# Kernel tuning notes

Hardware: AMD Instinct MI355X
Metric: run time of the kernel (lower is better)

## Reference

```python
import jax, jax.numpy as jnp
import numpy as np

N, T, C, K = 32, 1024, 512, 64
EPS = 1e-12  # torch F.normalize eps


def _l2norm(v, axis):
    n = jnp.sqrt(jnp.sum(v * v, axis=axis, keepdims=True))
    return v / jnp.maximum(n, EPS)


def setup_inputs() -> dict:
    key = jax.random.key(0)
    k1, k2 = jax.random.split(key)
    x = jax.random.normal(k1, (N, T, C), dtype=jnp.float32)
    centroids = jax.random.uniform(k2, (K, C), dtype=jnp.float32)
    # mirrors _init_params: conv.weight = 0.2*centroids, conv.bias = -0.1*||centroids||
    W = 0.2 * centroids
    b = -0.1 * jnp.sqrt(jnp.sum(centroids * centroids, axis=1))
    return {"x": x, "W": W, "b": b, "centroids": centroids}


def reference(x, W, b, centroids):
    # x: [N, T, C] -> [N, C, T]
    xt = jnp.transpose(x, (0, 2, 1))
    # 1x1 Conv1d == per-timestep linear: logits [N, K, T]
    logits = jnp.einsum('kc,nct->nkt', W, xt) + b[None, :, None]
    a = jax.nn.softmax(logits, axis=1)  # softmax over clusters
    # vlad[n,k,c] = sum_t a[n,k,t] * (x[n,c,t] - centroid[k,c])
    #            = (a @ x^T) - sum_t(a) * centroid  (GEMM form, same math)
    vlad = jnp.einsum('nkt,nct->nkc', a, xt) - a.sum(axis=-1)[:, :, None] * centroids[None]
    vlad = _l2norm(vlad, axis=2)          # intra-normalization per cluster
    vlad = vlad.reshape(vlad.shape[0], -1)
    vlad = _l2norm(vlad, axis=1)          # global L2 normalization
    return vlad
```

## Files before the change

### kernel.cpp

```cpp
#include <hip/hip_runtime.h>
#include <cmath>

namespace {

constexpr int N = 32, T = 1024, C = 512, K = 64;
constexpr float EPS = 1e-12f;

typedef short s8v __attribute__((ext_vector_type(8)));
typedef short s4v __attribute__((ext_vector_type(4)));
typedef float f4v __attribute__((ext_vector_type(4)));

__device__ inline unsigned short f2bh(float f) {
  __bf16 h = (__bf16)f;
  return __builtin_bit_cast(unsigned short, h);
}
__device__ inline float bh2f(unsigned short u) {
  __bf16 h = __builtin_bit_cast(__bf16, u);
  return (float)h;
}

#define MFMA16(A, B, Cc) __builtin_amdgcn_mfma_f32_16x16x32_bf16((A), (B), (Cc), 0, 0, 0)

__global__ __launch_bounds__(256, 4) void k_gemm1(
    const float* __restrict__ x, const float* __restrict__ W,
    const float* __restrict__ b, float* __restrict__ aT,
    float* __restrict__ asum_part) {
  __shared__ __align__(16) unsigned short sm[4 * 64 * 72];
  __shared__ float asum_l[256];
  unsigned short* xh_s = sm;
  unsigned short* xl_s = sm + 64 * 72;
  unsigned short* wh_s = sm + 2 * 64 * 72;
  unsigned short* wl_s = sm + 3 * 64 * 72;

  const int tid = threadIdx.x;
  const int w = tid >> 6, lane = tid & 63, lm = lane & 15, lq = lane >> 4;
  const int th = w >> 1;
  const int kh = w & 1;
  const long r0 = (long)blockIdx.x * 64;
  const int n = blockIdx.x >> 4, tl = blockIdx.x & 15;

  f4v acc[2][2] = {};
  float4 px[4], pw[4];
#pragma unroll
  for (int r = 0; r < 4; ++r) {
    const int f = tid + r * 256, t = f >> 4, cg = f & 15;
    px[r] = *(const float4*)&x[(r0 + t) * C + cg * 4];
    pw[r] = *(const float4*)&W[(long)t * C + cg * 4];
  }

  for (int c0 = 0; c0 < C; c0 += 64) {
    __syncthreads();
#pragma unroll
    for (int r = 0; r < 4; ++r) {
      const int f = tid + r * 256, t = f >> 4, cg = f & 15;
      const float ex[4] = {px[r].x, px[r].y, px[r].z, px[r].w};
      const float ew[4] = {pw[r].x, pw[r].y, pw[r].z, pw[r].w};
      s4v xh, xl, wh, wl;
#pragma unroll
      for (int i = 0; i < 4; ++i) {
        unsigned short hb = f2bh(ex[i]);
        xh[i] = (short)hb; xl[i] = (short)f2bh(ex[i] - bh2f(hb));
        hb = f2bh(ew[i]);
        wh[i] = (short)hb; wl[i] = (short)f2bh(ew[i] - bh2f(hb));
      }
      *(s4v*)&xh_s[t * 72 + cg * 4] = xh;
      *(s4v*)&xl_s[t * 72 + cg * 4] = xl;
      *(s4v*)&wh_s[t * 72 + cg * 4] = wh;
      *(s4v*)&wl_s[t * 72 + cg * 4] = wl;
    }
    if (c0 + 64 < C) {
#pragma unroll
      for (int r = 0; r < 4; ++r) {
        const int f = tid + r * 256, t = f >> 4, cg = f & 15;
        px[r] = *(const float4*)&x[(r0 + t) * C + c0 + 64 + cg * 4];
        pw[r] = *(const float4*)&W[(long)t * C + c0 + 64 + cg * 4];
      }
    }
    __syncthreads();

#pragma unroll
    for (int ks = 0; ks < 2; ++ks) {
      const int col = ks * 32 + lq * 8;
      s8v ah[2], al[2], bh[2], bl[2];
#pragma unroll
      for (int i = 0; i < 2; ++i) {
        ah[i] = *(const s8v*)&xh_s[(th * 32 + i * 16 + lm) * 72 + col];
        al[i] = *(const s8v*)&xl_s[(th * 32 + i * 16 + lm) * 72 + col];
        bh[i] = *(const s8v*)&wh_s[(kh * 32 + i * 16 + lm) * 72 + col];
        bl[i] = *(const s8v*)&wl_s[(kh * 32 + i * 16 + lm) * 72 + col];
      }
#pragma unroll
      for (int i = 0; i < 2; ++i)
#pragma unroll
        for (int j = 0; j < 2; ++j) {
          acc[i][j] = MFMA16(ah[i], bh[j], acc[i][j]);
          acc[i][j] = MFMA16(ah[i], bl[j], acc[i][j]);
          acc[i][j] = MFMA16(al[i], bh[j], acc[i][j]);
        }
    }
  }
  __syncthreads();

  float* Ls = (float*)sm;
  float* Ls2 = (float*)(sm + 8704);
  const float bias[2] = {b[kh * 32 + lm], b[kh * 32 + 16 + lm]};
#pragma unroll
  for (int i = 0; i < 2; ++i)
#pragma unroll
    for (int j = 0; j < 2; ++j)
#pragma unroll
      for (int r = 0; r < 4; ++r)
        Ls[(th * 32 + i * 16 + lq * 4 + r) * 68 + kh * 32 + j * 16 + lm] =
            acc[i][j][r] + bias[j];
  __syncthreads();

  {
    const int row = tid >> 2, q = tid & 3;
    float av[16];
#pragma unroll
    for (int u = 0; u < 4; ++u)
      *(float4*)&av[u * 4] = *(const float4*)&Ls[row * 68 + q * 16 + u * 4];
    float m = av[0];
#pragma unroll
    for (int i = 1; i < 16; ++i) m = fmaxf(m, av[i]);
    m = fmaxf(m, __shfl_xor(m, 1, 64));
    m = fmaxf(m, __shfl_xor(m, 2, 64));
    float sum = 0.f;
#pragma unroll
    for (int i = 0; i < 16; ++i) {
      av[i] = __expf(av[i] - m);
      sum += av[i];
    }
    sum += __shfl_xor(sum, 1, 64);
    sum += __shfl_xor(sum, 2, 64);
    const float inv = 1.f / sum;
    float ps[16];
#pragma unroll
    for (int i = 0; i < 16; ++i) {
      av[i] *= inv;
      ps[i] = av[i];
      Ls2[(q * 16 + i) * 68 + row] = av[i];
    }
#pragma unroll
    for (int s = 4; s < 64; s <<= 1)
#pragma unroll
      for (int i = 0; i < 16; ++i) ps[i] += __shfl_xor(ps[i], s, 64);
    if (lane < 4) {
#pragma unroll
      for (int i = 0; i < 16; ++i) asum_l[w * 64 + q * 16 + i] = ps[i];
    }
  }
  __syncthreads();

  if (tid < 64) {
    asum_part[(n * 16 + tl) * 64 + tid] = asum_l[tid] + asum_l[64 + tid] +
                                          asum_l[128 + tid] + asum_l[192 + tid];
  }
#pragma unroll
  for (int r = 0; r < 4; ++r) {
    const int u = tid + r * 256, k = u >> 4, tg = u & 15;
    *(float4*)&aT[((long)n * K + k) * T + tl * 64 + tg * 4] =
        *(const float4*)&Ls2[k * 68 + tg * 4];
  }
}

__global__ __launch_bounds__(256, 2) void k_gemm2(
    const float* __restrict__ x, const float* __restrict__ aT,
    const float* __restrict__ asum_part, const float* __restrict__ cent,
    float* __restrict__ vlad, float* __restrict__ ssq_part) {
  __shared__ __align__(16) unsigned short sm[4 * 64 * 72];
  __shared__ float asum_l[64];
  __shared__ float ssq_l[128];
  unsigned short* ah_s = sm;
  unsigned short* al_s = sm + 64 * 72;
  unsigned short* xh_s = sm + 2 * 64 * 72;
  unsigned short* xl_s = sm + 3 * 64 * 72;

  const int tid = threadIdx.x;
  const int w = tid >> 6, lane = tid & 63, lm = lane & 15, lq = lane >> 4;
  const int kh = w >> 1;
  const int ch = w & 1;
  const int n = blockIdx.x >> 3, cb = blockIdx.x & 7;
  const int c0 = cb * 64;

  if (tid < 64) {
    float s = 0.f;
#pragma unroll
    for (int tl = 0; tl < 16; ++tl) s += asum_part[(n * 16 + tl) * 64 + tid];
    asum_l[tid] = s;
  }

  f4v acc[2][2] = {};
  float4 pa[4], px[4];
#pragma unroll
  for (int r = 0; r < 4; ++r) {
    const int u = tid + r * 256, k = u >> 4, tg = u & 15;
    pa[r] = *(const float4*)&aT[((long)n * K + k) * T + tg * 4];
  }
  {
    const int cg = tid & 15, tq = tid >> 4;
#pragma unroll
    for (int i = 0; i < 4; ++i)
      px[i] = *(const float4*)&x[((long)n * T + tq * 4 + i) * C + c0 + cg * 4];
  }

  for (int t0 = 0; t0 < T; t0 += 64) {
    __syncthreads();
#pragma unroll
    for (int r = 0; r < 4; ++r) {
      const int u = tid + r * 256, k = u >> 4, tg = u & 15;
      const float e[4] = {pa[r].x, pa[r].y, pa[r].z, pa[r].w};
      s4v h, l;
#pragma unroll
      for (int i = 0; i < 4; ++i) {
        unsigned short hb = f2bh(e[i]);
        h[i] = (short)hb;
        l[i] = (short)f2bh(e[i] - bh2f(hb));
      }
      *(s4v*)&ah_s[k * 72 + tg * 4] = h;
      *(s4v*)&al_s[k * 72 + tg * 4] = l;
    }
    {
      const int cg = tid & 15, tq = tid >> 4, t4 = tq * 4;
      float e[4][4];
#pragma unroll
      for (int i = 0; i < 4; ++i) {
        e[i][0] = px[i].x; e[i][1] = px[i].y;
        e[i][2] = px[i].z; e[i][3] = px[i].w;
      }
#pragma unroll
      for (int cc = 0; cc < 4; ++cc) {
        s4v h, l;
#pragma unroll
        for (int i = 0; i < 4; ++i) {
          unsigned short hb = f2bh(e[i][cc]);
          h[i] = (short)hb;
          l[i] = (short)f2bh(e[i][cc] - bh2f(hb));
        }
        *(s4v*)&xh_s[(cg * 4 + cc) * 72 + t4] = h;
        *(s4v*)&xl_s[(cg * 4 + cc) * 72 + t4] = l;
      }
    }
    if (t0 + 64 < T) {
#pragma unroll
      for (int r = 0; r < 4; ++r) {
        const int u = tid + r * 256, k = u >> 4, tg = u & 15;
        pa[r] = *(const float4*)&aT[((long)n * K + k) * T + t0 + 64 + tg * 4];
      }
      const int cg = tid & 15, tq = tid >> 4;
#pragma unroll
      for (int i = 0; i < 4; ++i)
        px[i] = *(const float4*)&x[((long)n * T + t0 + 64 + tq * 4 + i) * C +
                                   c0 + cg * 4];
    }
    __syncthreads();

#pragma unroll
    for (int ks = 0; ks < 2; ++ks) {
      const int col = ks * 32 + lq * 8;
      s8v ah[2], al[2], bh[2], bl[2];
#pragma unroll
      for (int i = 0; i < 2; ++i) {
        ah[i] = *(const s8v*)&ah_s[(kh * 32 + i * 16 + lm) * 72 + col];
        al[i] = *(const s8v*)&al_s[(kh * 32 + i * 16 + lm) * 72 + col];
        bh[i] = *(const s8v*)&xh_s[(ch * 32 + i * 16 + lm) * 72 + col];
        bl[i] = *(const s8v*)&xl_s[(ch * 32 + i * 16 + lm) * 72 + col];
      }
#pragma unroll
      for (int i = 0; i < 2; ++i)
#pragma unroll
        for (int j = 0; j < 2; ++j) {
          acc[i][j] = MFMA16(ah[i], bh[j], acc[i][j]);
          acc[i][j] = MFMA16(ah[i], bl[j], acc[i][j]);
          acc[i][j] = MFMA16(al[i], bh[j], acc[i][j]);
        }
    }
  }

  float ssq[2][4];
#pragma unroll
  for (int i = 0; i < 2; ++i)
#pragma unroll
    for (int r = 0; r < 4; ++r) ssq[i][r] = 0.f;

#pragma unroll
  for (int i = 0; i < 2; ++i) {
#pragma unroll
    for (int r = 0; r < 4; ++r) {
      const int k = kh * 32 + i * 16 + lq * 4 + r;
      const float as = asum_l[k];
#pragma unroll
      for (int j = 0; j < 2; ++j) {
        const int c = c0 + ch * 32 + j * 16 + lm;
        const float v = acc[i][j][r] - as * cent[(long)k * C + c];
        vlad[((long)n * K + k) * C + c] = v;
        ssq[i][r] += v * v;
      }
    }
  }
#pragma unroll
  for (int i = 0; i < 2; ++i)
#pragma unroll
    for (int r = 0; r < 4; ++r) {
      float s = ssq[i][r];
      s += __shfl_xor(s, 1, 64);
      s += __shfl_xor(s, 2, 64);
      s += __shfl_xor(s, 4, 64);
      s += __shfl_xor(s, 8, 64);
      ssq[i][r] = s;
    }
  if (lm == 0) {
#pragma unroll
    for (int i = 0; i < 2; ++i)
#pragma unroll
      for (int r = 0; r < 4; ++r)
        ssq_l[(kh * 32 + i * 16 + lq * 4 + r) * 2 + ch] = ssq[i][r];
  }
  __syncthreads();
  if (tid < 64)
    ssq_part[(n * 8 + cb) * 64 + tid] = ssq_l[tid * 2] + ssq_l[tid * 2 + 1];
}

__global__ __launch_bounds__(256) void k_norm(
    const float* __restrict__ vlad, const float* __restrict__ ssq_part,
    float* __restrict__ out) {
  __shared__ float denom[64];
  __shared__ float contrib[64];
  __shared__ float ginv;

  const int tid = threadIdx.x;
  const int n = blockIdx.x >> 4;
  const int chunk = blockIdx.x & 15;

  if (tid < 64) {
    float ss = 0.f;
#pragma unroll
    for (int cb = 0; cb < 8; ++cb) ss += ssq_part[(n * 8 + cb) * 64 + tid];
    const float d = fmaxf(sqrtf(ss), EPS);
    denom[tid] = d;
    contrib[tid] = ss / (d * d);
  }
  __syncthreads();
  if (tid == 0) {
    float s = 0.f;
#pragma unroll
    for (int k = 0; k < K; ++k) s += contrib[k];
    ginv = 1.0f / fmaxf(sqrtf(s), EPS);
  }
  __syncthreads();

#pragma unroll
  for (int q = 0; q < 2; ++q) {
    const int f4 = tid + q * 256;
    const long off = chunk * 2048 + (long)f4 * 4;
    const int k = (int)(off >> 9);
    float4 v = *(const float4*)&vlad[(long)n * K * C + off];
    const float sc = ginv / denom[k];
    v.x *= sc; v.y *= sc; v.z *= sc; v.w *= sc;
    *(float4*)&out[(long)n * K * C + off] = v;
  }
}

}

extern "C" void kernel_launch(void* const* d_in, const int* in_sizes, int n_in,
                              void* d_out, int out_size, void* d_ws,
                              size_t ws_size, hipStream_t stream) {
  const float* x = reinterpret_cast<const float*>(d_in[0]);
  const float* W = reinterpret_cast<const float*>(d_in[1]);
  const float* b = reinterpret_cast<const float*>(d_in[2]);
  const float* cent = reinterpret_cast<const float*>(d_in[3]);
  float* out = reinterpret_cast<float*>(d_out);

  float* p = reinterpret_cast<float*>(d_ws);
  float* aTg = p;                 p += (size_t)N * K * T;
  float* vlad = p;                p += (size_t)N * K * C;
  float* asum_part = p;           p += (size_t)512 * 64;
  float* ssq_part = p;

  k_gemm1<<<(N * T) / 64, 256, 0, stream>>>(x, W, b, aTg, asum_part);
  k_gemm2<<<N * 8, 256, 0, stream>>>(x, aTg, asum_part, cent, vlad, ssq_part);
  k_norm<<<N * 16, 256, 0, stream>>>(vlad, ssq_part, out);
}
```

Baseline: 128.7 us.

## Double-buffer LDS with 32-wide K steps in both GEMM kernels

Both GEMM kernels now use two LDS buffers with a 32-element reduction step. Each iteration computes from one buffer while converting and storing the next tile into the other, so only one barrier per step is needed instead of two. In gemm2, thread roles are split so half the threads load x and half load the assignment matrix, which cuts registers per thread. This adds twice as many loop iterations, and gemm1's launch bound drops to 2 blocks per CU, which may reduce occupancy.

```diff
diff --git a/kernel.cpp b/kernel.cpp
--- a/kernel.cpp
+++ b/kernel.cpp
@@ -5,6 +5,8 @@
 
 constexpr int N = 32, T = 1024, C = 512, K = 64;
 constexpr float EPS = 1e-12f;
+constexpr int SR = 40;
+constexpr int PL = 64 * SR;
 
 typedef short s8v __attribute__((ext_vector_type(8)));
 typedef short s4v __attribute__((ext_vector_type(4)));
@@ -18,19 +20,24 @@
   __bf16 h = __builtin_bit_cast(__bf16, u);
   return (float)h;
 }
+__device__ inline void cvt4(const float4 v, s4v& h, s4v& l) {
+  const float e[4] = {v.x, v.y, v.z, v.w};
+#pragma unroll
+  for (int i = 0; i < 4; ++i) {
+    unsigned short hb = f2bh(e[i]);
+    h[i] = (short)hb;
+    l[i] = (short)f2bh(e[i] - bh2f(hb));
+  }
+}
 
 #define MFMA16(A, B, Cc) __builtin_amdgcn_mfma_f32_16x16x32_bf16((A), (B), (Cc), 0, 0, 0)
 
-__global__ __launch_bounds__(256, 4) void k_gemm1(
+__global__ __launch_bounds__(256, 2) void k_gemm1(
     const float* __restrict__ x, const float* __restrict__ W,
     const float* __restrict__ b, float* __restrict__ aT,
     float* __restrict__ asum_part) {
-  __shared__ __align__(16) unsigned short sm[4 * 64 * 72];
+  __shared__ __align__(16) unsigned short sm[2][4 * PL];
   __shared__ float asum_l[256];
-  unsigned short* xh_s = sm;
-  unsigned short* xl_s = sm + 64 * 72;
-  unsigned short* wh_s = sm + 2 * 64 * 72;
-  unsigned short* wl_s = sm + 3 * 64 * 72;
 
   const int tid = threadIdx.x;
   const int w = tid >> 6, lane = tid & 63, lm = lane & 15, lq = lane >> 4;
@@ -40,54 +47,56 @@
   const int n = blockIdx.x >> 4, tl = blockIdx.x & 15;
 
   f4v acc[2][2] = {};
-  float4 px[4], pw[4];
-#pragma unroll
-  for (int r = 0; r < 4; ++r) {
-    const int f = tid + r * 256, t = f >> 4, cg = f & 15;
+  float4 px[2], pw[2];
+
+#pragma unroll
+  for (int r = 0; r < 2; ++r) {
+    const int u = tid + r * 256, t = u >> 3, cg = u & 7;
     px[r] = *(const float4*)&x[(r0 + t) * C + cg * 4];
     pw[r] = *(const float4*)&W[(long)t * C + cg * 4];
   }
-
-  for (int c0 = 0; c0 < C; c0 += 64) {
-    __syncthreads();
-#pragma unroll
-    for (int r = 0; r < 4; ++r) {
-      const int f = tid + r * 256, t = f >> 4, cg = f & 15;
-      const float ex[4] = {px[r].x, px[r].y, px[r].z, px[r].w};
-      const float ew[4] = {pw[r].x, pw[r].y, pw[r].z, pw[r].w};
-      s4v xh, xl, wh, wl;
-#pragma unroll
-      for (int i = 0; i < 4; ++i) {
-        unsigned short hb = f2bh(ex[i]);
-        xh[i] = (short)hb; xl[i] = (short)f2bh(ex[i] - bh2f(hb));
-        hb = f2bh(ew[i]);
-        wh[i] = (short)hb; wl[i] = (short)f2bh(ew[i] - bh2f(hb));
-      }
-      *(s4v*)&xh_s[t * 72 + cg * 4] = xh;
-      *(s4v*)&xl_s[t * 72 + cg * 4] = xl;
-      *(s4v*)&wh_s[t * 72 + cg * 4] = wh;
-      *(s4v*)&wl_s[t * 72 + cg * 4] = wl;
-    }
-    if (c0 + 64 < C) {
-#pragma unroll
-      for (int r = 0; r < 4; ++r) {
-        const int f = tid + r * 256, t = f >> 4, cg = f & 15;
-        px[r] = *(const float4*)&x[(r0 + t) * C + c0 + 64 + cg * 4];
-        pw[r] = *(const float4*)&W[(long)t * C + c0 + 64 + cg * 4];
-      }
-    }
-    __syncthreads();
-
-#pragma unroll
-    for (int ks = 0; ks < 2; ++ks) {
-      const int col = ks * 32 + lq * 8;
+  {
+    unsigned short* xh = sm[0];
+    unsigned short* xl = sm[0] + PL;
+    unsigned short* wh = sm[0] + 2 * PL;
+    unsigned short* wl = sm[0] + 3 * PL;
+#pragma unroll
+    for (int r = 0; r < 2; ++r) {
+      const int u = tid + r * 256, t = u >> 3, cg = u & 7;
+      s4v h, l;
+      cvt4(px[r], h, l);
+      *(s4v*)&xh[t * SR + cg * 4] = h;
+      *(s4v*)&xl[t * SR + cg * 4] = l;
+      cvt4(pw[r], h, l);
+      *(s4v*)&wh[t * SR + cg * 4] = h;
+      *(s4v*)&wl[t * SR + cg * 4] = l;
+    }
+  }
+  __syncthreads();
+
+  for (int it = 0; it < 16; ++it) {
+    const int cur = it & 1;
+    if (it < 15) {
+      const int c0 = (it + 1) * 32;
+#pragma unroll
+      for (int r = 0; r < 2; ++r) {
+        const int u = tid + r * 256, t = u >> 3, cg = u & 7;
+        px[r] = *(const float4*)&x[(r0 + t) * C + c0 + cg * 4];
+        pw[r] = *(const float4*)&W[(long)t * C + c0 + cg * 4];
+      }
+    }
+    {
+      const unsigned short* xh = sm[cur];
+      const unsigned short* xl = sm[cur] + PL;
+      const unsigned short* wh = sm[cur] + 2 * PL;
+      const unsigned short* wl = sm[cur] + 3 * PL;
       s8v ah[2], al[2], bh[2], bl[2];
 #pragma unroll
       for (int i = 0; i < 2; ++i) {
-        ah[i] = *(const s8v*)&xh_s[(th * 32 + i * 16 + lm) * 72 + col];
-        al[i] = *(const s8v*)&xl_s[(th * 32 + i * 16 + lm) * 72 + col];
-        bh[i] = *(const s8v*)&wh_s[(kh * 32 + i * 16 + lm) * 72 + col];
-        bl[i] = *(const s8v*)&wl_s[(kh * 32 + i * 16 + lm) * 72 + col];
+        ah[i] = *(const s8v*)&xh[(th * 32 + i * 16 + lm) * SR + lq * 8];
+        al[i] = *(const s8v*)&xl[(th * 32 + i * 16 + lm) * SR + lq * 8];
+        bh[i] = *(const s8v*)&wh[(kh * 32 + i * 16 + lm) * SR + lq * 8];
+        bl[i] = *(const s8v*)&wl[(kh * 32 + i * 16 + lm) * SR + lq * 8];
       }
 #pragma unroll
       for (int i = 0; i < 2; ++i)
@@ -98,11 +107,28 @@
           acc[i][j] = MFMA16(al[i], bh[j], acc[i][j]);
         }
     }
-  }
-  __syncthreads();
-
-  float* Ls = (float*)sm;
-  float* Ls2 = (float*)(sm + 8704);
+    if (it < 15) {
+      unsigned short* xh = sm[cur ^ 1];
+      unsigned short* xl = sm[cur ^ 1] + PL;
+      unsigned short* wh = sm[cur ^ 1] + 2 * PL;
+      unsigned short* wl = sm[cur ^ 1] + 3 * PL;
+#pragma unroll
+      for (int r = 0; r < 2; ++r) {
+        const int u = tid + r * 256, t = u >> 3, cg = u & 7;
+        s4v h, l;
+        cvt4(px[r], h, l);
+        *(s4v*)&xh[t * SR + cg * 4] = h;
+        *(s4v*)&xl[t * SR + cg * 4] = l;
+        cvt4(pw[r], h, l);
+        *(s4v*)&wh[t * SR + cg * 4] = h;
+        *(s4v*)&wl[t * SR + cg * 4] = l;
+      }
+    }
+    __syncthreads();
+  }
+
+  float* Ls = (float*)&sm[0][0];
+  float* Ls2 = (float*)&sm[1][0];
   const float bias[2] = {b[kh * 32 + lm], b[kh * 32 + 16 + lm]};
 #pragma unroll
   for (int i = 0; i < 2; ++i)
@@ -168,13 +194,9 @@
     const float* __restrict__ x, const float* __restrict__ aT,
     const float* __restrict__ asum_part, const float* __restrict__ cent,
     float* __restrict__ vlad, float* __restrict__ ssq_part) {
-  __shared__ __align__(16) unsigned short sm[4 * 64 * 72];
+  __shared__ __align__(16) unsigned short sm[2][4 * PL];
   __shared__ float asum_l[64];
   __shared__ float ssq_l[128];
-  unsigned short* ah_s = sm;
-  unsigned short* al_s = sm + 64 * 72;
-  unsigned short* xh_s = sm + 2 * 64 * 72;
-  unsigned short* xl_s = sm + 3 * 64 * 72;
 
   const int tid = threadIdx.x;
   const int w = tid >> 6, lane = tid & 63, lm = lane & 15, lq = lane >> 4;
@@ -190,81 +212,81 @@
     asum_l[tid] = s;
   }
 
+  const bool xrole = (tid < 128);
+  const int xcg = tid & 15, xtq = (tid >> 4) & 7;
+  const int au = tid & 127, ak = au >> 1, atg = au & 1;
+
   f4v acc[2][2] = {};
-  float4 pa[4], px[4];
-#pragma unroll
-  for (int r = 0; r < 4; ++r) {
-    const int u = tid + r * 256, k = u >> 4, tg = u & 15;
-    pa[r] = *(const float4*)&aT[((long)n * K + k) * T + tg * 4];
+  float4 p[4];
+
+  if (xrole) {
+#pragma unroll
+    for (int i = 0; i < 4; ++i)
+      p[i] = *(const float4*)&x[((long)n * T + xtq * 4 + i) * C + c0 + xcg * 4];
+  } else {
+#pragma unroll
+    for (int q = 0; q < 4; ++q)
+      p[q] = *(const float4*)&aT[((long)n * K + ak) * T + atg * 16 + q * 4];
   }
   {
-    const int cg = tid & 15, tq = tid >> 4;
-#pragma unroll
-    for (int i = 0; i < 4; ++i)
-      px[i] = *(const float4*)&x[((long)n * T + tq * 4 + i) * C + c0 + cg * 4];
-  }
-
-  for (int t0 = 0; t0 < T; t0 += 64) {
-    __syncthreads();
-#pragma unroll
-    for (int r = 0; r < 4; ++r) {
-      const int u = tid + r * 256, k = u >> 4, tg = u & 15;
-      const float e[4] = {pa[r].x, pa[r].y, pa[r].z, pa[r].w};
-      s4v h, l;
-#pragma unroll
-      for (int i = 0; i < 4; ++i) {
-        unsigned short hb = f2bh(e[i]);
-        h[i] = (short)hb;
-        l[i] = (short)f2bh(e[i] - bh2f(hb));
-      }
-      *(s4v*)&ah_s[k * 72 + tg * 4] = h;
-      *(s4v*)&al_s[k * 72 + tg * 4] = l;
-    }
-    {
-      const int cg = tid & 15, tq = tid >> 4, t4 = tq * 4;
-      float e[4][4];
-#pragma unroll
-      for (int i = 0; i < 4; ++i) {
-        e[i][0] = px[i].x; e[i][1] = px[i].y;
-        e[i][2] = px[i].z; e[i][3] = px[i].w;
-      }
+    unsigned short* ah = sm[0];
+    unsigned short* al = sm[0] + PL;
+    unsigned short* xh = sm[0] + 2 * PL;
+    unsigned short* xl = sm[0] + 3 * PL;
+    if (xrole) {
 #pragma unroll
       for (int cc = 0; cc < 4; ++cc) {
         s4v h, l;
 #pragma unroll
         for (int i = 0; i < 4; ++i) {
-          unsigned short hb = f2bh(e[i][cc]);
+          const float e = ((const float*)&p[i])[cc];
+          unsigned short hb = f2bh(e);
           h[i] = (short)hb;
-          l[i] = (short)f2bh(e[i][cc] - bh2f(hb));
+          l[i] = (short)f2bh(e - bh2f(hb));
         }
-        *(s4v*)&xh_s[(cg * 4 + cc) * 72 + t4] = h;
-        *(s4v*)&xl_s[(cg * 4 + cc) * 72 + t4] = l;
-      }
-    }
-    if (t0 + 64 < T) {
-#pragma unroll
-      for (int r = 0; r < 4; ++r) {
-        const int u = tid + r * 256, k = u >> 4, tg = u & 15;
-        pa[r] = *(const float4*)&aT[((long)n * K + k) * T + t0 + 64 + tg * 4];
-      }
-      const int cg = tid & 15, tq = tid >> 4;
-#pragma unroll
-      for (int i = 0; i < 4; ++i)
-        px[i] = *(const float4*)&x[((long)n * T + t0 + 64 + tq * 4 + i) * C +
-                                   c0 + cg * 4];
-    }
-    __syncthreads();
-
-#pragma unroll
-    for (int ks = 0; ks < 2; ++ks) {
-      const int col = ks * 32 + lq * 8;
+        *(s4v*)&xh[(xcg * 4 + cc) * SR + xtq * 4] = h;
+        *(s4v*)&xl[(xcg * 4 + cc) * SR + xtq * 4] = l;
+      }
+    } else {
+#pragma unroll
+      for (int q = 0; q < 4; ++q) {
+        s4v h, l;
+        cvt4(p[q], h, l);
+        *(s4v*)&ah[ak * SR + atg * 16 + q * 4] = h;
+        *(s4v*)&al[ak * SR + atg * 16 + q * 4] = l;
+      }
+    }
+  }
+  __syncthreads();
+
+  for (int it = 0; it < 32; ++it) {
+    const int cur = it & 1;
+    if (it < 31) {
+      const int t0 = (it + 1) * 32;
+      if (xrole) {
+#pragma unroll
+        for (int i = 0; i < 4; ++i)
+          p[i] = *(const float4*)&x[((long)n * T + t0 + xtq * 4 + i) * C + c0 +
+                                    xcg * 4];
+      } else {
+#pragma unroll
+        for (int q = 0; q < 4; ++q)
+          p[q] =
+              *(const float4*)&aT[((long)n * K + ak) * T + t0 + atg * 16 + q * 4];
+      }
+    }
+    {
+      const unsigned short* ahp = sm[cur];
+      const unsigned short* alp = sm[cur] + PL;
+      const unsigned short* xhp = sm[cur] + 2 * PL;
+      const unsigned short* xlp = sm[cur] + 3 * PL;
       s8v ah[2], al[2], bh[2], bl[2];
 #pragma unroll
       for (int i = 0; i < 2; ++i) {
-        ah[i] = *(const s8v*)&ah_s[(kh * 32 + i * 16 + lm) * 72 + col];
-        al[i] = *(const s8v*)&al_s[(kh * 32 + i * 16 + lm) * 72 + col];
-        bh[i] = *(const s8v*)&xh_s[(ch * 32 + i * 16 + lm) * 72 + col];
-        bl[i] = *(const s8v*)&xl_s[(ch * 32 + i * 16 + lm) * 72 + col];
+        ah[i] = *(const s8v*)&ahp[(kh * 32 + i * 16 + lm) * SR + lq * 8];
+        al[i] = *(const s8v*)&alp[(kh * 32 + i * 16 + lm) * SR + lq * 8];
+        bh[i] = *(const s8v*)&xhp[(ch * 32 + i * 16 + lm) * SR + lq * 8];
+        bl[i] = *(const s8v*)&xlp[(ch * 32 + i * 16 + lm) * SR + lq * 8];
       }
 #pragma unroll
       for (int i = 0; i < 2; ++i)
@@ -275,6 +297,36 @@
           acc[i][j] = MFMA16(al[i], bh[j], acc[i][j]);
         }
     }
+    if (it < 31) {
+      unsigned short* ah = sm[cur ^ 1];
+      unsigned short* al = sm[cur ^ 1] + PL;
+      unsigned short* xh = sm[cur ^ 1] + 2 * PL;
+      unsigned short* xl = sm[cur ^ 1] + 3 * PL;
+      if (xrole) {
+#pragma unroll
+        for (int cc = 0; cc < 4; ++cc) {
+          s4v h, l;
+#pragma unroll
+          for (int i = 0; i < 4; ++i) {
+            const float e = ((const float*)&p[i])[cc];
+            unsigned short hb = f2bh(e);
+            h[i] = (short)hb;
+            l[i] = (short)f2bh(e - bh2f(hb));
+          }
+          *(s4v*)&xh[(xcg * 4 + cc) * SR + xtq * 4] = h;
+          *(s4v*)&xl[(xcg * 4 + cc) * SR + xtq * 4] = l;
+        }
+      } else {
+#pragma unroll
+        for (int q = 0; q < 4; ++q) {
+          s4v h, l;
+          cvt4(p[q], h, l);
+          *(s4v*)&ah[ak * SR + atg * 16 + q * 4] = h;
+          *(s4v*)&al[ak * SR + atg * 16 + q * 4] = l;
+        }
+      }
+    }
+    __syncthreads();
   }
 
   float ssq[2][4];
```

After: 171.7 us. 1.33x slower.

## Split gemm2 over two time halves and add a reduction/stat kernel

Applied to the files above, without the earlier changes.

The second GEMM is split along T into two halves, doubling the grid from 256 to 512 blocks so more CUs are busy. Each half writes raw partial sums to a workspace buffer. A new k_stat kernel adds the two partials, subtracts asum*centroid, writes vlad (reusing the aT buffer) and computes the per-cluster sums of squares. This trades extra global traffic for the partial buffers and one more kernel launch against better occupancy of the GPU.

```diff
diff --git a/kernel.cpp b/kernel.cpp
--- a/kernel.cpp
+++ b/kernel.cpp
@@ -166,11 +166,8 @@
 
 __global__ __launch_bounds__(256, 2) void k_gemm2(
     const float* __restrict__ x, const float* __restrict__ aT,
-    const float* __restrict__ asum_part, const float* __restrict__ cent,
-    float* __restrict__ vlad, float* __restrict__ ssq_part) {
+    float* __restrict__ part) {
   __shared__ __align__(16) unsigned short sm[4 * 64 * 72];
-  __shared__ float asum_l[64];
-  __shared__ float ssq_l[128];
   unsigned short* ah_s = sm;
   unsigned short* al_s = sm + 64 * 72;
   unsigned short* xh_s = sm + 2 * 64 * 72;
@@ -180,31 +177,28 @@
   const int w = tid >> 6, lane = tid & 63, lm = lane & 15, lq = lane >> 4;
   const int kh = w >> 1;
   const int ch = w & 1;
-  const int n = blockIdx.x >> 3, cb = blockIdx.x & 7;
+  const int n = blockIdx.x >> 4;
+  const int tc = (blockIdx.x >> 3) & 1;
+  const int cb = blockIdx.x & 7;
   const int c0 = cb * 64;
-
-  if (tid < 64) {
-    float s = 0.f;
-#pragma unroll
-    for (int tl = 0; tl < 16; ++tl) s += asum_part[(n * 16 + tl) * 64 + tid];
-    asum_l[tid] = s;
-  }
+  const int tbase = tc * (T / 2);
 
   f4v acc[2][2] = {};
   float4 pa[4], px[4];
 #pragma unroll
   for (int r = 0; r < 4; ++r) {
     const int u = tid + r * 256, k = u >> 4, tg = u & 15;
-    pa[r] = *(const float4*)&aT[((long)n * K + k) * T + tg * 4];
+    pa[r] = *(const float4*)&aT[((long)n * K + k) * T + tbase + tg * 4];
   }
   {
     const int cg = tid & 15, tq = tid >> 4;
 #pragma unroll
     for (int i = 0; i < 4; ++i)
-      px[i] = *(const float4*)&x[((long)n * T + tq * 4 + i) * C + c0 + cg * 4];
-  }
-
-  for (int t0 = 0; t0 < T; t0 += 64) {
+      px[i] = *(const float4*)&x[((long)n * T + tbase + tq * 4 + i) * C + c0 +
+                                 cg * 4];
+  }
+
+  for (int t0 = tbase; t0 < tbase + T / 2; t0 += 64) {
     __syncthreads();
 #pragma unroll
     for (int r = 0; r < 4; ++r) {
@@ -241,7 +235,7 @@
         *(s4v*)&xl_s[(cg * 4 + cc) * 72 + t4] = l;
       }
     }
-    if (t0 + 64 < T) {
+    if (t0 + 64 < tbase + T / 2) {
 #pragma unroll
       for (int r = 0; r < 4; ++r) {
         const int u = tid + r * 256, k = u >> 4, tg = u & 15;
@@ -277,52 +271,66 @@
     }
   }
 
-  float ssq[2][4];
+  float* pb = part + ((long)tc * N + n) * K * C;
 #pragma unroll
   for (int i = 0; i < 2; ++i)
 #pragma unroll
-    for (int r = 0; r < 4; ++r) ssq[i][r] = 0.f;
-
-#pragma unroll
-  for (int i = 0; i < 2; ++i) {
-#pragma unroll
-    for (int r = 0; r < 4; ++r) {
-      const int k = kh * 32 + i * 16 + lq * 4 + r;
-      const float as = asum_l[k];
-#pragma unroll
-      for (int j = 0; j < 2; ++j) {
+    for (int j = 0; j < 2; ++j)
+#pragma unroll
+      for (int r = 0; r < 4; ++r) {
+        const int k = kh * 32 + i * 16 + lq * 4 + r;
         const int c = c0 + ch * 32 + j * 16 + lm;
-        const float v = acc[i][j][r] - as * cent[(long)k * C + c];
-        vlad[((long)n * K + k) * C + c] = v;
-        ssq[i][r] += v * v;
-      }
-    }
-  }
-#pragma unroll
-  for (int i = 0; i < 2; ++i)
-#pragma unroll
-    for (int r = 0; r < 4; ++r) {
-      float s = ssq[i][r];
-      s += __shfl_xor(s, 1, 64);
-      s += __shfl_xor(s, 2, 64);
-      s += __shfl_xor(s, 4, 64);
-      s += __shfl_xor(s, 8, 64);
-      ssq[i][r] = s;
-    }
-  if (lm == 0) {
-#pragma unroll
-    for (int i = 0; i < 2; ++i)
-#pragma unroll
-      for (int r = 0; r < 4; ++r)
-        ssq_l[(kh * 32 + i * 16 + lq * 4 + r) * 2 + ch] = ssq[i][r];
-  }
-  __syncthreads();
-  if (tid < 64)
-    ssq_part[(n * 8 + cb) * 64 + tid] = ssq_l[tid * 2] + ssq_l[tid * 2 + 1];
+        pb[(long)k * C + c] = acc[i][j][r];
+      }
+}
+
+__global__ __launch_bounds__(256) void k_stat(
+    const float* __restrict__ part, const float* __restrict__ asum_part,
+    const float* __restrict__ cent, float* __restrict__ vlad,
+    float* __restrict__ ssq) {
+  __shared__ float asum_l[8];
+  __shared__ float ssq_l[8];
+  const int tid = threadIdx.x;
+  const int n = blockIdx.x >> 3;
+  const int kc = blockIdx.x & 7;
+
+  if (tid < 8) {
+    float s = 0.f;
+#pragma unroll
+    for (int tl = 0; tl < 16; ++tl)
+      s += asum_part[(n * 16 + tl) * 64 + kc * 8 + tid];
+    asum_l[tid] = s;
+  }
+  __syncthreads();
+
+  const int kl = tid >> 5;
+  const float as = asum_l[kl];
+  const long Lb = (long)kc * 4096 + tid * 16;
+  const long nb = (long)n * K * C;
+
+  float ss = 0.f;
+#pragma unroll
+  for (int q = 0; q < 4; ++q) {
+    const float4 p0 = *(const float4*)&part[nb + Lb + q * 4];
+    const float4 p1 = *(const float4*)&part[(long)N * K * C + nb + Lb + q * 4];
+    const float4 cv = *(const float4*)&cent[Lb + q * 4];
+    float4 v;
+    v.x = p0.x + p1.x - as * cv.x;
+    v.y = p0.y + p1.y - as * cv.y;
+    v.z = p0.z + p1.z - as * cv.z;
+    v.w = p0.w + p1.w - as * cv.w;
+    *(float4*)&vlad[nb + Lb + q * 4] = v;
+    ss += v.x * v.x + v.y * v.y + v.z * v.z + v.w * v.w;
+  }
+#pragma unroll
+  for (int s = 1; s < 32; s <<= 1) ss += __shfl_xor(ss, s, 64);
+  if ((tid & 31) == 0) ssq_l[kl] = ss;
+  __syncthreads();
+  if (tid < 8) ssq[n * K + kc * 8 + tid] = ssq_l[tid];
 }
 
 __global__ __launch_bounds__(256) void k_norm(
-    const float* __restrict__ vlad, const float* __restrict__ ssq_part,
+    const float* __restrict__ vlad, const float* __restrict__ ssq,
     float* __restrict__ out) {
   __shared__ float denom[64];
   __shared__ float contrib[64];
@@ -333,12 +341,10 @@
   const int chunk = blockIdx.x & 15;
 
   if (tid < 64) {
-    float ss = 0.f;
-#pragma unroll
-    for (int cb = 0; cb < 8; ++cb) ss += ssq_part[(n * 8 + cb) * 64 + tid];
-    const float d = fmaxf(sqrtf(ss), EPS);
+    const float sv = ssq[n * K + tid];
+    const float d = fmaxf(sqrtf(sv), EPS);
     denom[tid] = d;
-    contrib[tid] = ss / (d * d);
+    contrib[tid] = sv / (d * d);
   }
   __syncthreads();
   if (tid == 0) {
@@ -374,11 +380,13 @@
 
   float* p = reinterpret_cast<float*>(d_ws);
   float* aTg = p;                 p += (size_t)N * K * T;
-  float* vlad = p;                p += (size_t)N * K * C;
+  float* part = p;                p += (size_t)2 * N * K * C;
   float* asum_part = p;           p += (size_t)512 * 64;
-  float* ssq_part = p;
+  float* ssq = p;                 p += (size_t)N * K;
+  float* vlad = aTg;
 
   k_gemm1<<<(N * T) / 64, 256, 0, stream>>>(x, W, b, aTg, asum_part);
-  k_gemm2<<<N * 8, 256, 0, stream>>>(x, aTg, asum_part, cent, vlad, ssq_part);
-  k_norm<<<N * 16, 256, 0, stream>>>(vlad, ssq_part, out);
-}
+  k_gemm2<<<N * 16, 256, 0, stream>>>(x, aTg, part);
+  k_stat<<<N * 8, 256, 0, stream>>>(part, asum_part, cent, vlad, ssq);
+  k_norm<<<N * 16, 256, 0, stream>>>(vlad, ssq, out);
+}
```

Measured after the change: 132.9 us. +3.2%, slower.

## Fuse normalization into gemm2 via atomic grid barrier; store attention pre-split bf16

Applied to the files above, without the earlier changes.

Removes the separate normalization kernel and the vlad intermediate buffer. gemm2 now accumulates per-cluster sums of squares with atomics, waits on a per-batch counter spin barrier over its 8 blocks, and then scales its register-resident results directly into the output. gemm1 also writes the attention matrix already split into bf16 high and low halves, so gemm2 skips the conversion and loads half-width data. The spin barrier assumes all 8 blocks of each batch are co-resident, which holds for 256 blocks at 2 per CU. It adds atomic and spin-wait latency in return.

```diff
diff --git a/kernel.cpp b/kernel.cpp
--- a/kernel.cpp
+++ b/kernel.cpp
@@ -23,8 +23,9 @@
 
 __global__ __launch_bounds__(256, 4) void k_gemm1(
     const float* __restrict__ x, const float* __restrict__ W,
-    const float* __restrict__ b, float* __restrict__ aT,
-    float* __restrict__ asum_part) {
+    const float* __restrict__ b, unsigned short* __restrict__ ath,
+    unsigned short* __restrict__ atl, float* __restrict__ asum_part,
+    float* __restrict__ ssq, unsigned int* __restrict__ counter) {
   __shared__ __align__(16) unsigned short sm[4 * 64 * 72];
   __shared__ float asum_l[256];
   unsigned short* xh_s = sm;
@@ -39,6 +40,12 @@
   const long r0 = (long)blockIdx.x * 64;
   const int n = blockIdx.x >> 4, tl = blockIdx.x & 15;
 
+  if (blockIdx.x == 0) {
+    if (tid < 32) counter[tid] = 0u;
+#pragma unroll
+    for (int q = 0; q < 8; ++q) ssq[tid * 8 + q] = 0.f;
+  }
+
   f4v acc[2][2] = {};
   float4 px[4], pw[4];
 #pragma unroll
@@ -159,18 +166,32 @@
 #pragma unroll
   for (int r = 0; r < 4; ++r) {
     const int u = tid + r * 256, k = u >> 4, tg = u & 15;
-    *(float4*)&aT[((long)n * K + k) * T + tl * 64 + tg * 4] =
-        *(const float4*)&Ls2[k * 68 + tg * 4];
+    const float4 v = *(const float4*)&Ls2[k * 68 + tg * 4];
+    const float e[4] = {v.x, v.y, v.z, v.w};
+    s4v h, l;
+#pragma unroll
+    for (int i = 0; i < 4; ++i) {
+      unsigned short hb = f2bh(e[i]);
+      h[i] = (short)hb;
+      l[i] = (short)f2bh(e[i] - bh2f(hb));
+    }
+    *(s4v*)&ath[((long)n * K + k) * T + tl * 64 + tg * 4] = h;
+    *(s4v*)&atl[((long)n * K + k) * T + tl * 64 + tg * 4] = l;
   }
 }
 
 __global__ __launch_bounds__(256, 2) void k_gemm2(
-    const float* __restrict__ x, const float* __restrict__ aT,
+    const float* __restrict__ x, const unsigned short* __restrict__ ath,
+    const unsigned short* __restrict__ atl,
     const float* __restrict__ asum_part, const float* __restrict__ cent,
-    float* __restrict__ vlad, float* __restrict__ ssq_part) {
+    float* __restrict__ ssq, unsigned int* __restrict__ counter,
+    float* __restrict__ out) {
   __shared__ __align__(16) unsigned short sm[4 * 64 * 72];
   __shared__ float asum_l[64];
   __shared__ float ssq_l[128];
+  __shared__ float denom_l[64];
+  __shared__ float contrib_l[64];
+  __shared__ float ginv_s;
   unsigned short* ah_s = sm;
   unsigned short* al_s = sm + 64 * 72;
   unsigned short* xh_s = sm + 2 * 64 * 72;
@@ -191,11 +212,13 @@
   }
 
   f4v acc[2][2] = {};
-  float4 pa[4], px[4];
-#pragma unroll
-  for (int r = 0; r < 4; ++r) {
-    const int u = tid + r * 256, k = u >> 4, tg = u & 15;
-    pa[r] = *(const float4*)&aT[((long)n * K + k) * T + tg * 4];
+  s8v pah[2], pal[2];
+  float4 px[4];
+#pragma unroll
+  for (int r = 0; r < 2; ++r) {
+    const int u = tid + r * 256, k = u >> 3, tg = u & 7;
+    pah[r] = *(const s8v*)&ath[((long)n * K + k) * T + tg * 8];
+    pal[r] = *(const s8v*)&atl[((long)n * K + k) * T + tg * 8];
   }
   {
     const int cg = tid & 15, tq = tid >> 4;
@@ -207,35 +230,22 @@
   for (int t0 = 0; t0 < T; t0 += 64) {
     __syncthreads();
 #pragma unroll
-    for (int r = 0; r < 4; ++r) {
-      const int u = tid + r * 256, k = u >> 4, tg = u & 15;
-      const float e[4] = {pa[r].x, pa[r].y, pa[r].z, pa[r].w};
-      s4v h, l;
-#pragma unroll
-      for (int i = 0; i < 4; ++i) {
-        unsigned short hb = f2bh(e[i]);
-        h[i] = (short)hb;
-        l[i] = (short)f2bh(e[i] - bh2f(hb));
-      }
-      *(s4v*)&ah_s[k * 72 + tg * 4] = h;
-      *(s4v*)&al_s[k * 72 + tg * 4] = l;
+    for (int r = 0; r < 2; ++r) {
+      const int u = tid + r * 256, k = u >> 3, tg = u & 7;
+      *(s8v*)&ah_s[k * 72 + tg * 8] = pah[r];
+      *(s8v*)&al_s[k * 72 + tg * 8] = pal[r];
     }
     {
       const int cg = tid & 15, tq = tid >> 4, t4 = tq * 4;
-      float e[4][4];
-#pragma unroll
-      for (int i = 0; i < 4; ++i) {
-        e[i][0] = px[i].x; e[i][1] = px[i].y;
-        e[i][2] = px[i].z; e[i][3] = px[i].w;
-      }
 #pragma unroll
       for (int cc = 0; cc < 4; ++cc) {
         s4v h, l;
 #pragma unroll
         for (int i = 0; i < 4; ++i) {
-          unsigned short hb = f2bh(e[i][cc]);
+          const float e = ((const float*)&px[i])[cc];
+          unsigned short hb = f2bh(e);
           h[i] = (short)hb;
-          l[i] = (short)f2bh(e[i][cc] - bh2f(hb));
+          l[i] = (short)f2bh(e - bh2f(hb));
         }
         *(s4v*)&xh_s[(cg * 4 + cc) * 72 + t4] = h;
         *(s4v*)&xl_s[(cg * 4 + cc) * 72 + t4] = l;
@@ -243,9 +253,10 @@
     }
     if (t0 + 64 < T) {
 #pragma unroll
-      for (int r = 0; r < 4; ++r) {
-        const int u = tid + r * 256, k = u >> 4, tg = u & 15;
-        pa[r] = *(const float4*)&aT[((long)n * K + k) * T + t0 + 64 + tg * 4];
+      for (int r = 0; r < 2; ++r) {
+        const int u = tid + r * 256, k = u >> 3, tg = u & 7;
+        pah[r] = *(const s8v*)&ath[((long)n * K + k) * T + t0 + 64 + tg * 8];
+        pal[r] = *(const s8v*)&atl[((long)n * K + k) * T + t0 + 64 + tg * 8];
       }
       const int cg = tid & 15, tq = tid >> 4;
 #pragma unroll
@@ -277,11 +288,11 @@
     }
   }
 
-  float ssq[2][4];
+  float ssqp[2][4];
 #pragma unroll
   for (int i = 0; i < 2; ++i)
 #pragma unroll
-    for (int r = 0; r < 4; ++r) ssq[i][r] = 0.f;
+    for (int r = 0; r < 4; ++r) ssqp[i][r] = 0.f;
 
 #pragma unroll
   for (int i = 0; i < 2; ++i) {
@@ -293,8 +304,8 @@
       for (int j = 0; j < 2; ++j) {
         const int c = c0 + ch * 32 + j * 16 + lm;
         const float v = acc[i][j][r] - as * cent[(long)k * C + c];
-        vlad[((long)n * K + k) * C + c] = v;
-        ssq[i][r] += v * v;
+        acc[i][j][r] = v;
+        ssqp[i][r] += v * v;
       }
     }
   }
@@ -302,63 +313,63 @@
   for (int i = 0; i < 2; ++i)
 #pragma unroll
     for (int r = 0; r < 4; ++r) {
-      float s = ssq[i][r];
+      float s = ssqp[i][r];
       s += __shfl_xor(s, 1, 64);
       s += __shfl_xor(s, 2, 64);
       s += __shfl_xor(s, 4, 64);
       s += __shfl_xor(s, 8, 64);
-      ssq[i][r] = s;
+      ssqp[i][r] = s;
     }
   if (lm == 0) {
 #pragma unroll
     for (int i = 0; i < 2; ++i)
 #pragma unroll
       for (int r = 0; r < 4; ++r)
-        ssq_l[(kh * 32 + i * 16 + lq * 4 + r) * 2 + ch] = ssq[i][r];
-  }
-  __syncthreads();
-  if (tid < 64)
-    ssq_part[(n * 8 + cb) * 64 + tid] = ssq_l[tid * 2] + ssq_l[tid * 2 + 1];
-}
-
-__global__ __launch_bounds__(256) void k_norm(
-    const float* __restrict__ vlad, const float* __restrict__ ssq_part,
-    float* __restrict__ out) {
-  __shared__ float denom[64];
-  __shared__ float contrib[64];
-  __shared__ float ginv;
-
-  const int tid = threadIdx.x;
-  const int n = blockIdx.x >> 4;
-  const int chunk = blockIdx.x & 15;
+        ssq_l[(kh * 32 + i * 16 + lq * 4 + r) * 2 + ch] = ssqp[i][r];
+  }
+  __syncthreads();
+  if (tid < 64) atomicAdd(&ssq[n * K + tid], ssq_l[tid * 2] + ssq_l[tid * 2 + 1]);
+  __threadfence();
+  __syncthreads();
+
+  if (tid == 0) {
+    atomicAdd(&counter[n], 1u);
+    while (__hip_atomic_load(&counter[n], __ATOMIC_RELAXED,
+                             __HIP_MEMORY_SCOPE_AGENT) < 8u)
+      __builtin_amdgcn_s_sleep(8);
+  }
+  __syncthreads();
+  __threadfence();
 
   if (tid < 64) {
-    float ss = 0.f;
-#pragma unroll
-    for (int cb = 0; cb < 8; ++cb) ss += ssq_part[(n * 8 + cb) * 64 + tid];
-    const float d = fmaxf(sqrtf(ss), EPS);
-    denom[tid] = d;
-    contrib[tid] = ss / (d * d);
+    const float sv = __hip_atomic_load(&ssq[n * K + tid], __ATOMIC_RELAXED,
+                                       __HIP_MEMORY_SCOPE_AGENT);
+    const float d = fmaxf(sqrtf(sv), EPS);
+    denom_l[tid] = d;
+    contrib_l[tid] = sv / (d * d);
   }
   __syncthreads();
   if (tid == 0) {
     float s = 0.f;
 #pragma unroll
-    for (int k = 0; k < K; ++k) s += contrib[k];
-    ginv = 1.0f / fmaxf(sqrtf(s), EPS);
-  }
-  __syncthreads();
-
-#pragma unroll
-  for (int q = 0; q < 2; ++q) {
-    const int f4 = tid + q * 256;
-    const long off = chunk * 2048 + (long)f4 * 4;
-    const int k = (int)(off >> 9);
-    float4 v = *(const float4*)&vlad[(long)n * K * C + off];
-    const float sc = ginv / denom[k];
-    v.x *= sc; v.y *= sc; v.z *= sc; v.w *= sc;
-    *(float4*)&out[(long)n * K * C + off] = v;
-  }
+    for (int k = 0; k < K; ++k) s += contrib_l[k];
+    ginv_s = 1.0f / fmaxf(sqrtf(s), EPS);
+  }
+  __syncthreads();
+
+  const float gi = ginv_s;
+#pragma unroll
+  for (int i = 0; i < 2; ++i)
+#pragma unroll
+    for (int r = 0; r < 4; ++r) {
+      const int k = kh * 32 + i * 16 + lq * 4 + r;
+      const float sc = gi / denom_l[k];
+#pragma unroll
+      for (int j = 0; j < 2; ++j) {
+        const int c = c0 + ch * 32 + j * 16 + lm;
+        out[((long)n * K + k) * C + c] = acc[i][j][r] * sc;
+      }
+    }
 }
 
 }
@@ -372,13 +383,15 @@
   const float* cent = reinterpret_cast<const float*>(d_in[3]);
   float* out = reinterpret_cast<float*>(d_out);
 
-  float* p = reinterpret_cast<float*>(d_ws);
-  float* aTg = p;                 p += (size_t)N * K * T;
-  float* vlad = p;                p += (size_t)N * K * C;
-  float* asum_part = p;           p += (size_t)512 * 64;
-  float* ssq_part = p;
-
-  k_gemm1<<<(N * T) / 64, 256, 0, stream>>>(x, W, b, aTg, asum_part);
-  k_gemm2<<<N * 8, 256, 0, stream>>>(x, aTg, asum_part, cent, vlad, ssq_part);
-  k_norm<<<N * 16, 256, 0, stream>>>(vlad, ssq_part, out);
-}
+  char* p = (char*)d_ws;
+  unsigned short* ath = (unsigned short*)p;  p += (size_t)N * K * T * 2;
+  unsigned short* atl = (unsigned short*)p;  p += (size_t)N * K * T * 2;
+  float* asum_part = (float*)p;              p += (size_t)512 * 64 * 4;
+  float* ssq = (float*)p;                    p += (size_t)N * K * 4;
+  unsigned int* counter = (unsigned int*)p;
+
+  k_gemm1<<<(N * T) / 64, 256, 0, stream>>>(x, W, b, ath, atl, asum_part, ssq,
+                                            counter);
+  k_gemm2<<<N * 8, 256, 0, stream>>>(x, ath, atl, asum_part, cent, ssq, counter,
+                                     out);
+}
```

Result: slower. 163.8 us (+27.3%).
